# Kernel optimization log

Measured on AMD Instinct MI355X. Metric: run time of the kernel, lower is better.

The kernel has to match this reference:

```python
import jax, jax.numpy as jnp
import numpy as np

B = 256        # batch_size = y.size(0)
N_BLK = 128    # n: nodes per perturbed subgraph (== hidden_channels so trace blocks are square)
C = 128        # hidden_channels
WALK = 7       # self.walk_len
N_P = B * N_BLK
E_P = N_P * 16
N_NP = N_BLK
E_NP = N_NP * 16


def _gcn_norm(edge_index, num_nodes):
    # PyG gcn_norm: add self loops, symmetric D^{-1/2} (A+I) D^{-1/2}
    loop = jnp.arange(num_nodes, dtype=edge_index.dtype)
    src = jnp.concatenate([edge_index[0], loop])
    dst = jnp.concatenate([edge_index[1], loop])
    deg = jax.ops.segment_sum(jnp.ones_like(dst, dtype=jnp.float32), dst, num_segments=num_nodes)
    dinv = jnp.where(deg > 0, jax.lax.rsqrt(deg), 0.0)
    norm = dinv[src] * dinv[dst]  # [E + N]
    return src, dst, norm


def _gcn(x, src, dst, norm, W, b, num_nodes):
    # GCNConv: aggregate normalized messages from src at dst of (x @ W), then + bias
    xw = x @ W
    out = jax.ops.segment_sum(xw[src] * norm[:, None], dst, num_segments=num_nodes)
    return out + b


def setup_inputs() -> dict:
    key = jax.random.key(0)
    ks = jax.random.split(key, 12)
    x_p = jax.random.normal(ks[0], (N_P, C), dtype=jnp.float32)
    x_np = jax.random.normal(ks[1], (N_NP, C), dtype=jnp.float32)
    y = jax.random.uniform(ks[2], (B, 1), dtype=jnp.float32)
    edge_index_p = jax.random.randint(ks[3], (2, E_P), 0, N_P, dtype=jnp.int64)
    edge_index_np = jax.random.randint(ks[4], (2, E_NP), 0, N_NP, dtype=jnp.int64)
    # shared GCNConv weight/bias (same self.wrnn.conv1 applied every step to both graphs)
    W_gcn = jax.random.normal(ks[5], (C, C), dtype=jnp.float32) / np.sqrt(C)
    b_gcn = jnp.zeros((C,), dtype=jnp.float32)
    # MLP: walk_len -> 15 -> 1
    W1 = jax.random.normal(ks[6], (WALK, 15), dtype=jnp.float32) / np.sqrt(WALK)
    b1 = jnp.zeros((15,), dtype=jnp.float32)
    W2 = jax.random.normal(ks[7], (15, 1), dtype=jnp.float32) / np.sqrt(15)
    b2 = jnp.zeros((1,), dtype=jnp.float32)
    return {"x_p": x_p, "x_np": x_np, "y": y,
            "edge_index_p": edge_index_p, "edge_index_np": edge_index_np,
            "W_gcn": W_gcn, "b_gcn": b_gcn,
            "W1": W1, "b1": b1, "W2": W2, "b2": b2}


def reference(x_p, x_np, y, edge_index_p, edge_index_np, W_gcn, b_gcn, W1, b1, W2, b2):
    src_p, dst_p, norm_p = _gcn_norm(edge_index_p, N_P)
    src_n, dst_n, norm_n = _gcn_norm(edge_index_np, N_NP)
    h_p, h_np = x_p, x_np
    p_traces, np_traces = [], []
    for _ in range(WALK):  # small fixed walk_len loop
        h_p = _gcn(h_p, src_p, dst_p, norm_p, W_gcn, b_gcn, N_P)
        h_np = _gcn(h_np, src_n, dst_n, norm_n, W_gcn, b_gcn, N_NP)
        np_traces.append(jnp.trace(h_np))
        # fused batched block-trace: trace of each [n, C] block (n == C)
        p_traces.append(jnp.einsum('bkk->b', h_p.reshape(B, N_BLK, C)))
    p_list = jnp.stack(p_traces, axis=1)          # [B, WALK]
    np_list = jnp.stack(np_traces)[None, :]       # [1, WALK] broadcast == repeat
    p_list = (p_list - np_list) * ((y - 0.5) * 2.0)  # per-row sign scale
    mu = jnp.mean(p_list, axis=0, keepdims=True)
    std = jnp.std(p_list, axis=0, keepdims=True, ddof=1)  # torch.std uses ddof=1
    p_list = (p_list - mu) / std
    h = jax.nn.relu(p_list @ W1 + b1)
    return jax.nn.sigmoid(h @ W2 + b2)            # [B, 1]
```

## Files before the change

### kernel.cpp

```cpp
#include <hip/hip_runtime.h>
#include <hip/hip_bf16.h>
#include <math.h>

namespace {

constexpr int C_DIM  = 128;
constexpr int B_SZ   = 256;
constexpr int NP_OFF = 32768;
constexpr int N_TOT  = 32896;
constexpr int E_P    = 524288;
constexpr int E_NP   = 2048;
constexpr int E_TOT  = E_P + E_NP;
constexpr int WALK   = 7;
constexpr int NTR    = 257;
constexpr int ESZ    = E_TOT + N_TOT;
constexpr int EPAD   = 64;


__device__ __forceinline__ float bflo(unsigned int w) { return __uint_as_float(w << 16); }
__device__ __forceinline__ float bfhi(unsigned int w) { return __uint_as_float(w & 0xffff0000u); }


__global__ void init_kernel(int* __restrict__ cnt, float* __restrict__ trG,
                            float* __restrict__ ctr, float* __restrict__ c0,
                            int* __restrict__ bflag,
                            unsigned* __restrict__ srcs, float* __restrict__ norms) {
  int i = blockIdx.x * blockDim.x + threadIdx.x;
  if (i < N_TOT) { cnt[i] = 0; c0[i] = 1.0f; }
  if (i < WALK * NTR) { trG[i] = 0.0f; ctr[i] = 0.0f; }
  if (i < EPAD) { srcs[ESZ + i] = 0u; norms[ESZ + i] = 0.0f; }
  if (i == 0) *bflag = 0;
}

__global__ void count_kernel(const int* __restrict__ ei_p,
                             const int* __restrict__ ei_np,
                             int* __restrict__ cnt) {
  int e = blockIdx.x * blockDim.x + threadIdx.x;
  if (e < E_P) {
    int d = ei_p[E_P + e];
    atomicAdd(&cnt[d], 1);
  } else if (e < E_TOT) {
    int i = e - E_P;
    int d = ei_np[E_NP + i] + NP_OFF;
    atomicAdd(&cnt[d], 1);
  }
}

__global__ void scan_kernel(const int* __restrict__ cnt, int* __restrict__ ptr) {
  const int T = 1024;
  __shared__ int part[T];
  int tid = threadIdx.x;
  const int chunk = (N_TOT + T - 1) / T;
  int begin = tid * chunk;
  int end = begin + chunk;
  if (end > N_TOT) end = N_TOT;
  int s = 0;
  for (int i = begin; i < end; ++i) s += cnt[i] + 1;
  part[tid] = s;
  __syncthreads();
  for (int off = 1; off < T; off <<= 1) {
    int v = (tid >= off) ? part[tid - off] : 0;
    __syncthreads();
    part[tid] += v;
    __syncthreads();
  }
  if (tid == T - 1) ptr[N_TOT] = part[T - 1];
  int run = (tid == 0) ? 0 : part[tid - 1];
  for (int i = begin; i < end; ++i) { ptr[i] = run; run += cnt[i] + 1; }
}

__global__ void dinv_kernel(const int* __restrict__ cnt, const int* __restrict__ ptr,
                            float* __restrict__ dinv, int* __restrict__ fill,
                            unsigned* __restrict__ srcs, float* __restrict__ norms) {
  int i = blockIdx.x * blockDim.x + threadIdx.x;
  if (i < N_TOT) {
    float di = rsqrtf((float)cnt[i] + 1.0f);
    dinv[i] = di;
    fill[i] = 0;
    int p = ptr[i];
    srcs[p] = (unsigned)i;
    norms[p] = di * di;
  }
}

__global__ void fill_kernel(const int* __restrict__ ei_p,
                            const int* __restrict__ ei_np,
                            const int* __restrict__ ptr, int* __restrict__ fill,
                            const float* __restrict__ dinv,
                            unsigned* __restrict__ srcs, float* __restrict__ norms) {
  int e = blockIdx.x * blockDim.x + threadIdx.x;
  int s, d;
  if (e < E_P) {
    s = ei_p[e];
    d = ei_p[E_P + e];
  } else if (e < E_TOT) {
    int i = e - E_P;
    s = ei_np[i] + NP_OFF;
    d = ei_np[E_NP + i] + NP_OFF;
  } else {
    return;
  }
  int k = atomicAdd(&fill[d], 1);
  if (k < 63) {
    int pos = ptr[d] + 1 + k;
    srcs[pos] = (unsigned)s;
    norms[pos] = dinv[s] * dinv[d];
  }
}

__global__ void concat_kernel(const float* __restrict__ x_p,
                              const float* __restrict__ x_np,
                              __hip_bfloat16* __restrict__ hb) {
  int i = blockIdx.x * blockDim.x + threadIdx.x;
  const int NP8 = NP_OFF * C_DIM / 8;
  const int NT8 = N_TOT * C_DIM / 8;
  if (i >= NT8) return;
  const float* src = (i < NP8) ? (x_p + (size_t)i * 8)
                               : (x_np + (size_t)(i - NP8) * 8);
  union { __hip_bfloat16 h[8]; uint4 u; } pk;
#pragma unroll
  for (int j = 0; j < 8; ++j) pk.h[j] = __float2bfloat16(src[j]);
  ((uint4*)hb)[i] = pk.u;
}

__global__ __launch_bounds__(128) void wpow_all_kernel(
    const float* __restrict__ W, float* __restrict__ Vt_all,
    float* __restrict__ dvec_all, const float* __restrict__ bg,
    int* __restrict__ bflag) {
  __shared__ float cur[C_DIM];
  const int i = blockIdx.x;
  const int j = threadIdx.x;
  if (i < C_DIM) {
    float u = W[i * C_DIM + j];
    Vt_all[0 * C_DIM * C_DIM + j * C_DIM + i] = u;
    for (int st = 1; st < WALK; ++st) {
      cur[j] = u;
      __syncthreads();
      float nu = 0.0f;
      for (int k = 0; k < C_DIM; ++k) nu += cur[k] * W[k * C_DIM + j];
      __syncthreads();
      u = nu;
      Vt_all[st * C_DIM * C_DIM + j * C_DIM + i] = u;
    }
  } else {
    float d = bg[j];
    if (d != 0.0f) atomicOr(bflag, 1);
    dvec_all[0 * C_DIM + j] = d;
    for (int st = 1; st < WALK; ++st) {
      cur[j] = d;
      __syncthreads();
      float nd = 0.0f;
      for (int k = 0; k < C_DIM; ++k) nd += cur[k] * W[k * C_DIM + j];
      __syncthreads();
      d = nd;
      dvec_all[st * C_DIM + j] = d;
    }
  }
}

__global__ __launch_bounds__(256) void step_kernel(
    const __hip_bfloat16* __restrict__ Gin,
    __hip_bfloat16* __restrict__ Gout,
    const int* __restrict__ ptr,
    const unsigned* __restrict__ srcs,
    const float* __restrict__ norms,
    const float* __restrict__ cin,
    float* __restrict__ cout,
    const float* __restrict__ Vt,
    const float* __restrict__ dvec,
    float* __restrict__ trG,
    float* __restrict__ ctr,
    const int* __restrict__ bflag,
    int st, int notlast) {
  const int lane = threadIdx.x & 63;
  const int wv   = threadIdx.x >> 6;
  const int q    = lane >> 4;
  const int c8   = lane & 15;
  const int base = (blockIdx.x * 4 + wv) * 16;
  const int n0   = base + 4 * q;
  const int n1   = n0 + 1;
  const int n2   = n0 + 2;
  const int n3   = n0 + 3;
  const int qb   = q << 4;

  const int p0 = ptr[n0];
  const int p1 = ptr[n1];
  const int p2 = ptr[n2];
  const int p3 = ptr[n3];
  int d0 = ptr[n0 + 1] - p0; if (d0 > 64) d0 = 64;
  int d1 = ptr[n1 + 1] - p1; if (d1 > 64) d1 = 64;
  int d2 = ptr[n2 + 1] - p2; if (d2 > 64) d2 = 64;
  int d3 = ptr[n3 + 1] - p3; if (d3 > 64) d3 = 64;
  int dmax = d0 > d1 ? d0 : d1;
  dmax = dmax > d2 ? dmax : d2;
  dmax = dmax > d3 ? dmax : d3;

  const unsigned* S0 = srcs + p0;   const float* F0 = norms + p0;
  const unsigned* S1 = srcs + p1;   const float* F1 = norms + p1;
  const unsigned* S2 = srcs + p2;   const float* F2 = norms + p2;
  const unsigned* S3 = srcs + p3;   const float* F3 = norms + p3;
  unsigned sA0 = S0[c8], sB0 = S0[16 + c8], sC0 = S0[32 + c8], sD0 = S0[48 + c8];
  float    nA0 = F0[c8], nB0 = F0[16 + c8], nC0 = F0[32 + c8], nD0 = F0[48 + c8];
  unsigned sA1 = S1[c8], sB1 = S1[16 + c8], sC1 = S1[32 + c8], sD1 = S1[48 + c8];
  float    nA1 = F1[c8], nB1 = F1[16 + c8], nC1 = F1[32 + c8], nD1 = F1[48 + c8];
  unsigned sA2 = S2[c8], sB2 = S2[16 + c8], sC2 = S2[32 + c8], sD2 = S2[48 + c8];
  float    nA2 = F2[c8], nB2 = F2[16 + c8], nC2 = F2[32 + c8], nD2 = F2[48 + c8];
  unsigned sA3 = S3[c8], sB3 = S3[16 + c8], sC3 = S3[32 + c8], sD3 = S3[48 + c8];
  float    nA3 = F3[c8], nB3 = F3[16 + c8], nC3 = F3[32 + c8], nD3 = F3[48 + c8];

  const uint4* __restrict__ G16 = (const uint4*)Gin;

  float acc0[8], acc1[8], acc2[8], acc3[8];
#pragma unroll
  for (int i = 0; i < 8; ++i) { acc0[i] = 0.0f; acc1[i] = 0.0f;
                                acc2[i] = 0.0f; acc3[i] = 0.0f; }

#define LOADN(K, SX, NX, DK)                                                   \
    unsigned x##K##a = __shfl(SX, qb + rr * 4 + 0);                            \
    unsigned x##K##b = __shfl(SX, qb + rr * 4 + 1);                            \
    unsigned x##K##c = __shfl(SX, qb + rr * 4 + 2);                            \
    unsigned x##K##d = __shfl(SX, qb + rr * 4 + 3);                            \
    float w##K##a = __shfl(NX, qb + rr * 4 + 0);                               \
    float w##K##b = __shfl(NX, qb + rr * 4 + 1);                               \
    float w##K##c = __shfl(NX, qb + rr * 4 + 2);                               \
    float w##K##d = __shfl(NX, qb + rr * 4 + 3);                               \
    w##K##a = (j0 + 0 < DK) ? w##K##a : 0.0f;                                  \
    w##K##b = (j0 + 1 < DK) ? w##K##b : 0.0f;                                  \
    w##K##c = (j0 + 2 < DK) ? w##K##c : 0.0f;                                  \
    w##K##d = (j0 + 3 < DK) ? w##K##d : 0.0f;                                  \
    x##K##a = x##K##a < N_TOT ? x##K##a : 0u;                                  \
    x##K##b = x##K##b < N_TOT ? x##K##b : 0u;                                  \
    x##K##c = x##K##c < N_TOT ? x##K##c : 0u;                                  \
    x##K##d = x##K##d < N_TOT ? x##K##d : 0u;                                  \
    uint4 g##K##a = G16[(size_t)x##K##a * 16 + c8];                            \
    uint4 g##K##b = G16[(size_t)x##K##b * 16 + c8];                            \
    uint4 g##K##c = G16[(size_t)x##K##c * 16 + c8];                            \
    uint4 g##K##d = G16[(size_t)x##K##d * 16 + c8];

#define CONSN(K, ACC)                                                          \
    ACC[0] += w##K##a * bflo(g##K##a.x) + w##K##b * bflo(g##K##b.x)            \
            + w##K##c * bflo(g##K##c.x) + w##K##d * bflo(g##K##d.x);           \
    ACC[1] += w##K##a * bfhi(g##K##a.x) + w##K##b * bfhi(g##K##b.x)            \
            + w##K##c * bfhi(g##K##c.x) + w##K##d * bfhi(g##K##d.x);           \
    ACC[2] += w##K##a * bflo(g##K##a.y) + w##K##b * bflo(g##K##b.y)            \
            + w##K##c * bflo(g##K##c.y) + w##K##d * bflo(g##K##d.y);           \
    ACC[3] += w##K##a * bfhi(g##K##a.y) + w##K##b * bfhi(g##K##b.y)            \
            + w##K##c * bfhi(g##K##c.y) + w##K##d * bfhi(g##K##d.y);           \
    ACC[4] += w##K##a * bflo(g##K##a.z) + w##K##b * bflo(g##K##b.z)            \
            + w##K##c * bflo(g##K##c.z) + w##K##d * bflo(g##K##d.z);           \
    ACC[5] += w##K##a * bfhi(g##K##a.z) + w##K##b * bfhi(g##K##b.z)            \
            + w##K##c * bfhi(g##K##c.z) + w##K##d * bfhi(g##K##d.z);           \
    ACC[6] += w##K##a * bflo(g##K##a.w) + w##K##b * bflo(g##K##b.w)            \
            + w##K##c * bflo(g##K##c.w) + w##K##d * bflo(g##K##d.w);           \
    ACC[7] += w##K##a * bfhi(g##K##a.w) + w##K##b * bfhi(g##K##b.w)            \
            + w##K##c * bfhi(g##K##c.w) + w##K##d * bfhi(g##K##d.w);

#define GROUP4(SX0, NX0, SX1, NX1, SX2, NX2, SX3, NX3, RG)                     \
  if ((RG) * 16 < dmax) {                                                      \
    for (int rr = 0; rr < 4; ++rr) {                                           \
      const int j0 = (RG) * 16 + rr * 4;                                       \
      if (j0 >= dmax) break;                                                   \
      LOADN(0, SX0, NX0, d0)                                                   \
      LOADN(1, SX1, NX1, d1)                                                   \
      LOADN(2, SX2, NX2, d2)                                                   \
      LOADN(3, SX3, NX3, d3)                                                   \
      CONSN(0, acc0)                                                           \
      CONSN(1, acc1)                                                           \
      CONSN(2, acc2)                                                           \
      CONSN(3, acc3)                                                           \
    }                                                                          \
  }

  GROUP4(sA0, nA0, sA1, nA1, sA2, nA2, sA3, nA3, 0)
  GROUP4(sB0, nB0, sB1, nB1, sB2, nB2, sB3, nB3, 1)
  GROUP4(sC0, nC0, sC1, nC1, sC2, nC2, sC3, nC3, 2)
  GROUP4(sD0, nD0, sD1, nD1, sD2, nD2, sD3, nD3, 3)
#undef GROUP4
#undef CONSN
#undef LOADN

  if (notlast) {
    union { __hip_bfloat16 h[8]; uint4 u; } pk0, pk1, pk2, pk3;
#pragma unroll
    for (int i = 0; i < 8; ++i) { pk0.h[i] = __float2bfloat16(acc0[i]);
                                  pk1.h[i] = __float2bfloat16(acc1[i]);
                                  pk2.h[i] = __float2bfloat16(acc2[i]);
                                  pk3.h[i] = __float2bfloat16(acc3[i]); }
    ((uint4*)Gout)[(size_t)n0 * 16 + c8] = pk0.u;
    ((uint4*)Gout)[(size_t)n1 * 16 + c8] = pk1.u;
    ((uint4*)Gout)[(size_t)n2 * 16 + c8] = pk2.u;
    ((uint4*)Gout)[(size_t)n3 * 16 + c8] = pk3.u;
  }

  const int col0 = n0 & 127, col1 = n1 & 127, col2 = n2 & 127, col3 = n3 & 127;
  const float4* vr0 = (const float4*)(Vt + col0 * C_DIM + c8 * 8);
  const float4* vr1 = (const float4*)(Vt + col1 * C_DIM + c8 * 8);
  const float4* vr2 = (const float4*)(Vt + col2 * C_DIM + c8 * 8);
  const float4* vr3 = (const float4*)(Vt + col3 * C_DIM + c8 * 8);
  const float4 v00 = vr0[0], v01 = vr0[1];
  const float4 v10 = vr1[0], v11 = vr1[1];
  const float4 v20 = vr2[0], v21 = vr2[1];
  const float4 v30 = vr3[0], v31 = vr3[1];
  float pd = acc0[0] * v00.x + acc0[1] * v00.y + acc0[2] * v00.z + acc0[3] * v00.w +
             acc0[4] * v01.x + acc0[5] * v01.y + acc0[6] * v01.z + acc0[7] * v01.w;
  pd      += acc1[0] * v10.x + acc1[1] * v10.y + acc1[2] * v10.z + acc1[3] * v10.w +
             acc1[4] * v11.x + acc1[5] * v11.y + acc1[6] * v11.z + acc1[7] * v11.w;
  pd      += acc2[0] * v20.x + acc2[1] * v20.y + acc2[2] * v20.z + acc2[3] * v20.w +
             acc2[4] * v21.x + acc2[5] * v21.y + acc2[6] * v21.z + acc2[7] * v21.w;
  pd      += acc3[0] * v30.x + acc3[1] * v30.y + acc3[2] * v30.z + acc3[3] * v30.w +
             acc3[4] * v31.x + acc3[5] * v31.y + acc3[6] * v31.z + acc3[7] * v31.w;
  pd += __shfl_xor(pd, 1);
  pd += __shfl_xor(pd, 2);
  pd += __shfl_xor(pd, 4);
  pd += __shfl_xor(pd, 8);

  const int bnz = *bflag;
  if (c8 == 0) {
    atomicAdd(&trG[st * NTR + (n0 >> 7)], pd);
    if (bnz) {
      float cs0 = cin[n0], cn0 = 0.0f;
      for (int e = 0; e < d0; ++e) cn0 += norms[p0 + e] * cin[srcs[p0 + e]];
      float cs1 = cin[n1], cn1 = 0.0f;
      for (int e = 0; e < d1; ++e) cn1 += norms[p1 + e] * cin[srcs[p1 + e]];
      float cs2 = cin[n2], cn2 = 0.0f;
      for (int e = 0; e < d2; ++e) cn2 += norms[p2 + e] * cin[srcs[p2 + e]];
      float cs3 = cin[n3], cn3 = 0.0f;
      for (int e = 0; e < d3; ++e) cn3 += norms[p3 + e] * cin[srcs[p3 + e]];
      if (notlast) { cout[n0] = cn0; cout[n1] = cn1;
                     cout[n2] = cn2; cout[n3] = cn3; }
      atomicAdd(&ctr[st * NTR + (n0 >> 7)],
                cs0 * dvec[col0] + cs1 * dvec[col1] +
                cs2 * dvec[col2] + cs3 * dvec[col3]);
    }
  }
}

__global__ __launch_bounds__(256) void final_kernel(const float* __restrict__ trG,
                                                    const float* __restrict__ ctr,
                                                    const float* __restrict__ y,
                                                    const float* __restrict__ W1,
                                                    const float* __restrict__ b1,
                                                    const float* __restrict__ W2,
                                                    const float* __restrict__ b2,
                                                    float* __restrict__ out) {
  __shared__ float sm[B_SZ];
  const int b = threadIdx.x;
  const float sgn = (y[b] - 0.5f) * 2.0f;
  float runb = 0.0f, runn = 0.0f;
  float vals[WALK];
#pragma unroll
  for (int t = 0; t < WALK; ++t) {
    runb += ctr[t * NTR + b];
    runn += ctr[t * NTR + 256];
    vals[t] = ((trG[t * NTR + b] + runb) - (trG[t * NTR + 256] + runn)) * sgn;
  }

  for (int t = 0; t < WALK; ++t) {
    sm[b] = vals[t];
    __syncthreads();
    for (int off = 128; off >= 1; off >>= 1) {
      if (b < off) sm[b] += sm[b + off];
      __syncthreads();
    }
    float mean = sm[0] * (1.0f / 256.0f);
    __syncthreads();
    float d = vals[t] - mean;
    sm[b] = d * d;
    __syncthreads();
    for (int off = 128; off >= 1; off >>= 1) {
      if (b < off) sm[b] += sm[b + off];
      __syncthreads();
    }
    float stdv = sqrtf(sm[0] * (1.0f / 255.0f));
    __syncthreads();
    vals[t] = d / stdv;
  }

  float o = b2[0];
#pragma unroll
  for (int j = 0; j < 15; ++j) {
    float a = b1[j];
#pragma unroll
    for (int t = 0; t < WALK; ++t) a += vals[t] * W1[t * 15 + j];
    o += fmaxf(a, 0.0f) * W2[j];
  }
  out[b] = 1.0f / (1.0f + expf(-o));
}

}

extern "C" void kernel_launch(void* const* d_in, const int* in_sizes, int n_in,
                              void* d_out, int out_size, void* d_ws, size_t ws_size,
                              hipStream_t stream) {
  const float* x_p   = (const float*)d_in[0];
  const float* x_np  = (const float*)d_in[1];
  const float* y     = (const float*)d_in[2];
  const int* ei_p    = (const int*)d_in[3];
  const int* ei_np   = (const int*)d_in[4];
  const float* W_gcn = (const float*)d_in[5];
  const float* b_gcn = (const float*)d_in[6];
  const float* W1    = (const float*)d_in[7];
  const float* b1    = (const float*)d_in[8];
  const float* W2    = (const float*)d_in[9];
  const float* b2    = (const float*)d_in[10];
  float* out         = (float*)d_out;

  char* p = (char*)d_ws;
  auto alloc = [&](size_t bytes) -> void* {
    void* r = (void*)p;
    p += (bytes + 255) & ~(size_t)255;
    return r;
  };
  __hip_bfloat16* Ga = (__hip_bfloat16*)alloc((size_t)N_TOT * C_DIM * 2);
  __hip_bfloat16* Gb = (__hip_bfloat16*)alloc((size_t)N_TOT * C_DIM * 2);
  unsigned* srcs  = (unsigned*)alloc((size_t)(ESZ + EPAD) * 4);
  float* norms    = (float*)alloc((size_t)(ESZ + EPAD) * 4);
  int*   ptr      = (int*)alloc((size_t)(N_TOT + 1) * 4);
  float* dinv     = (float*)alloc((size_t)N_TOT * 4);
  int*   cnt      = (int*)alloc((size_t)N_TOT * 4);
  int*   fill     = (int*)alloc((size_t)N_TOT * 4);
  float* ca       = (float*)alloc((size_t)N_TOT * 4);
  float* cb       = (float*)alloc((size_t)N_TOT * 4);
  float* Vt_all   = (float*)alloc((size_t)WALK * C_DIM * C_DIM * 4);
  float* dvec_all = (float*)alloc((size_t)WALK * C_DIM * 4);
  float* trG      = (float*)alloc((size_t)WALK * NTR * 4);
  float* ctr      = (float*)alloc((size_t)WALK * NTR * 4);
  int*   bflag    = (int*)alloc(4);

  init_kernel<<<(N_TOT + 255) / 256, 256, 0, stream>>>(cnt, trG, ctr, ca, bflag,
                                                       srcs, norms);
  count_kernel<<<(E_TOT + 255) / 256, 256, 0, stream>>>(ei_p, ei_np, cnt);
  scan_kernel<<<1, 1024, 0, stream>>>(cnt, ptr);
  dinv_kernel<<<(N_TOT + 255) / 256, 256, 0, stream>>>(cnt, ptr, dinv, fill,
                                                       srcs, norms);
  fill_kernel<<<(E_TOT + 255) / 256, 256, 0, stream>>>(ei_p, ei_np, ptr, fill,
                                                       dinv, srcs, norms);
  {
    const int NT8 = N_TOT * C_DIM / 8;
    concat_kernel<<<(NT8 + 255) / 256, 256, 0, stream>>>(x_p, x_np, Ga);
  }
  wpow_all_kernel<<<C_DIM + 1, C_DIM, 0, stream>>>(W_gcn, Vt_all, dvec_all,
                                                   b_gcn, bflag);

  __hip_bfloat16 *Gcur = Ga, *Gnext = Gb;
  float *ccur = ca, *cnext = cb;
  for (int st = 0; st < WALK; ++st) {
    const int notlast = (st < WALK - 1) ? 1 : 0;
    step_kernel<<<N_TOT / 64, 256, 0, stream>>>(Gcur, Gnext, ptr, srcs, norms,
                                                ccur, cnext,
                                                Vt_all + (size_t)st * C_DIM * C_DIM,
                                                dvec_all + (size_t)st * C_DIM,
                                                trG, ctr, bflag, st, notlast);
    { __hip_bfloat16* t = Gcur; Gcur = Gnext; Gnext = t; }
    { float* t = ccur; ccur = cnext; cnext = t; }
  }

  final_kernel<<<1, B_SZ, 0, stream>>>(trG, ctr, y, W1, b1, W2, b2, out);
}
```

Measured before the change: 476.3 us.

## Replace CSR adjacency with fixed-width ELL layout and drop the scan kernel

Adjacency is now stored in an ELL layout, a fixed 64-slot row per node indexed by node*64, instead of CSR with a prefix-sum pointer array. This removes the single-block scan kernel and the ptr loads in the step kernel. Edge index and norm loads for each 16-slot group are now issued only when that group is needed. The final kernel's tree reductions are replaced with wavefront shuffle reductions. The ELL buffers are larger (N*64 entries) and their rows are strided, which may cost memory traffic and coalescing.

```diff
diff --git a/kernel.cpp b/kernel.cpp
--- a/kernel.cpp
+++ b/kernel.cpp
@@ -13,8 +13,7 @@
 constexpr int E_TOT  = E_P + E_NP;
 constexpr int WALK   = 7;
 constexpr int NTR    = 257;
-constexpr int ESZ    = E_TOT + N_TOT;
-constexpr int EPAD   = 64;
+constexpr int ELLW   = 64;
 
 
 __device__ __forceinline__ float bflo(unsigned int w) { return __uint_as_float(w << 16); }
@@ -23,12 +22,10 @@
 
 __global__ void init_kernel(int* __restrict__ cnt, float* __restrict__ trG,
                             float* __restrict__ ctr, float* __restrict__ c0,
-                            int* __restrict__ bflag,
-                            unsigned* __restrict__ srcs, float* __restrict__ norms) {
+                            int* __restrict__ bflag) {
   int i = blockIdx.x * blockDim.x + threadIdx.x;
   if (i < N_TOT) { cnt[i] = 0; c0[i] = 1.0f; }
   if (i < WALK * NTR) { trG[i] = 0.0f; ctr[i] = 0.0f; }
-  if (i < EPAD) { srcs[ESZ + i] = 0u; norms[ESZ + i] = 0.0f; }
   if (i == 0) *bflag = 0;
 }
 
@@ -46,30 +43,7 @@
   }
 }
 
-__global__ void scan_kernel(const int* __restrict__ cnt, int* __restrict__ ptr) {
-  const int T = 1024;
-  __shared__ int part[T];
-  int tid = threadIdx.x;
-  const int chunk = (N_TOT + T - 1) / T;
-  int begin = tid * chunk;
-  int end = begin + chunk;
-  if (end > N_TOT) end = N_TOT;
-  int s = 0;
-  for (int i = begin; i < end; ++i) s += cnt[i] + 1;
-  part[tid] = s;
-  __syncthreads();
-  for (int off = 1; off < T; off <<= 1) {
-    int v = (tid >= off) ? part[tid - off] : 0;
-    __syncthreads();
-    part[tid] += v;
-    __syncthreads();
-  }
-  if (tid == T - 1) ptr[N_TOT] = part[T - 1];
-  int run = (tid == 0) ? 0 : part[tid - 1];
-  for (int i = begin; i < end; ++i) { ptr[i] = run; run += cnt[i] + 1; }
-}
-
-__global__ void dinv_kernel(const int* __restrict__ cnt, const int* __restrict__ ptr,
+__global__ void dinv_kernel(const int* __restrict__ cnt,
                             float* __restrict__ dinv, int* __restrict__ fill,
                             unsigned* __restrict__ srcs, float* __restrict__ norms) {
   int i = blockIdx.x * blockDim.x + threadIdx.x;
@@ -77,7 +51,7 @@
     float di = rsqrtf((float)cnt[i] + 1.0f);
     dinv[i] = di;
     fill[i] = 0;
-    int p = ptr[i];
+    size_t p = (size_t)i * ELLW;
     srcs[p] = (unsigned)i;
     norms[p] = di * di;
   }
@@ -85,7 +59,7 @@
 
 __global__ void fill_kernel(const int* __restrict__ ei_p,
                             const int* __restrict__ ei_np,
-                            const int* __restrict__ ptr, int* __restrict__ fill,
+                            int* __restrict__ fill,
                             const float* __restrict__ dinv,
                             unsigned* __restrict__ srcs, float* __restrict__ norms) {
   int e = blockIdx.x * blockDim.x + threadIdx.x;
@@ -101,8 +75,8 @@
     return;
   }
   int k = atomicAdd(&fill[d], 1);
-  if (k < 63) {
-    int pos = ptr[d] + 1 + k;
+  if (k < ELLW - 1) {
+    size_t pos = (size_t)d * ELLW + 1 + k;
     srcs[pos] = (unsigned)s;
     norms[pos] = dinv[s] * dinv[d];
   }
@@ -161,7 +135,7 @@
 __global__ __launch_bounds__(256) void step_kernel(
     const __hip_bfloat16* __restrict__ Gin,
     __hip_bfloat16* __restrict__ Gout,
-    const int* __restrict__ ptr,
+    const int* __restrict__ cnt,
     const unsigned* __restrict__ srcs,
     const float* __restrict__ norms,
     const float* __restrict__ cin,
@@ -183,30 +157,18 @@
   const int n3   = n0 + 3;
   const int qb   = q << 4;
 
-  const int p0 = ptr[n0];
-  const int p1 = ptr[n1];
-  const int p2 = ptr[n2];
-  const int p3 = ptr[n3];
-  int d0 = ptr[n0 + 1] - p0; if (d0 > 64) d0 = 64;
-  int d1 = ptr[n1 + 1] - p1; if (d1 > 64) d1 = 64;
-  int d2 = ptr[n2 + 1] - p2; if (d2 > 64) d2 = 64;
-  int d3 = ptr[n3 + 1] - p3; if (d3 > 64) d3 = 64;
+  int d0 = cnt[n0] + 1; if (d0 > ELLW) d0 = ELLW;
+  int d1 = cnt[n1] + 1; if (d1 > ELLW) d1 = ELLW;
+  int d2 = cnt[n2] + 1; if (d2 > ELLW) d2 = ELLW;
+  int d3 = cnt[n3] + 1; if (d3 > ELLW) d3 = ELLW;
   int dmax = d0 > d1 ? d0 : d1;
   dmax = dmax > d2 ? dmax : d2;
   dmax = dmax > d3 ? dmax : d3;
 
-  const unsigned* S0 = srcs + p0;   const float* F0 = norms + p0;
-  const unsigned* S1 = srcs + p1;   const float* F1 = norms + p1;
-  const unsigned* S2 = srcs + p2;   const float* F2 = norms + p2;
-  const unsigned* S3 = srcs + p3;   const float* F3 = norms + p3;
-  unsigned sA0 = S0[c8], sB0 = S0[16 + c8], sC0 = S0[32 + c8], sD0 = S0[48 + c8];
-  float    nA0 = F0[c8], nB0 = F0[16 + c8], nC0 = F0[32 + c8], nD0 = F0[48 + c8];
-  unsigned sA1 = S1[c8], sB1 = S1[16 + c8], sC1 = S1[32 + c8], sD1 = S1[48 + c8];
-  float    nA1 = F1[c8], nB1 = F1[16 + c8], nC1 = F1[32 + c8], nD1 = F1[48 + c8];
-  unsigned sA2 = S2[c8], sB2 = S2[16 + c8], sC2 = S2[32 + c8], sD2 = S2[48 + c8];
-  float    nA2 = F2[c8], nB2 = F2[16 + c8], nC2 = F2[32 + c8], nD2 = F2[48 + c8];
-  unsigned sA3 = S3[c8], sB3 = S3[16 + c8], sC3 = S3[32 + c8], sD3 = S3[48 + c8];
-  float    nA3 = F3[c8], nB3 = F3[16 + c8], nC3 = F3[32 + c8], nD3 = F3[48 + c8];
+  const unsigned* S0 = srcs + (size_t)n0 * ELLW;  const float* F0 = norms + (size_t)n0 * ELLW;
+  const unsigned* S1 = srcs + (size_t)n1 * ELLW;  const float* F1 = norms + (size_t)n1 * ELLW;
+  const unsigned* S2 = srcs + (size_t)n2 * ELLW;  const float* F2 = norms + (size_t)n2 * ELLW;
+  const unsigned* S3 = srcs + (size_t)n3 * ELLW;  const float* F3 = norms + (size_t)n3 * ELLW;
 
   const uint4* __restrict__ G16 = (const uint4*)Gin;
 
@@ -256,7 +218,7 @@
             + w##K##c * bfhi(g##K##c.w) + w##K##d * bfhi(g##K##d.w);
 
 #define GROUP4(SX0, NX0, SX1, NX1, SX2, NX2, SX3, NX3, RG)                     \
-  if ((RG) * 16 < dmax) {                                                      \
+  {                                                                            \
     for (int rr = 0; rr < 4; ++rr) {                                           \
       const int j0 = (RG) * 16 + rr * 4;                                       \
       if (j0 >= dmax) break;                                                   \
@@ -271,10 +233,26 @@
     }                                                                          \
   }
 
-  GROUP4(sA0, nA0, sA1, nA1, sA2, nA2, sA3, nA3, 0)
-  GROUP4(sB0, nB0, sB1, nB1, sB2, nB2, sB3, nB3, 1)
-  GROUP4(sC0, nC0, sC1, nC1, sC2, nC2, sC3, nC3, 2)
-  GROUP4(sD0, nD0, sD1, nD1, sD2, nD2, sD3, nD3, 3)
+  {
+    unsigned sA0 = S0[c8], sA1 = S1[c8], sA2 = S2[c8], sA3 = S3[c8];
+    float    nA0 = F0[c8], nA1 = F1[c8], nA2 = F2[c8], nA3 = F3[c8];
+    unsigned sB0 = S0[16 + c8], sB1 = S1[16 + c8], sB2 = S2[16 + c8], sB3 = S3[16 + c8];
+    float    nB0 = F0[16 + c8], nB1 = F1[16 + c8], nB2 = F2[16 + c8], nB3 = F3[16 + c8];
+    GROUP4(sA0, nA0, sA1, nA1, sA2, nA2, sA3, nA3, 0)
+    if (16 < dmax) {
+      GROUP4(sB0, nB0, sB1, nB1, sB2, nB2, sB3, nB3, 1)
+    }
+  }
+  if (32 < dmax) {
+    unsigned sC0 = S0[32 + c8], sC1 = S1[32 + c8], sC2 = S2[32 + c8], sC3 = S3[32 + c8];
+    float    nC0 = F0[32 + c8], nC1 = F1[32 + c8], nC2 = F2[32 + c8], nC3 = F3[32 + c8];
+    GROUP4(sC0, nC0, sC1, nC1, sC2, nC2, sC3, nC3, 2)
+    if (48 < dmax) {
+      unsigned sD0 = S0[48 + c8], sD1 = S1[48 + c8], sD2 = S2[48 + c8], sD3 = S3[48 + c8];
+      float    nD0 = F0[48 + c8], nD1 = F1[48 + c8], nD2 = F2[48 + c8], nD3 = F3[48 + c8];
+      GROUP4(sD0, nD0, sD1, nD1, sD2, nD2, sD3, nD3, 3)
+    }
+  }
 #undef GROUP4
 #undef CONSN
 #undef LOADN
@@ -319,13 +297,13 @@
     atomicAdd(&trG[st * NTR + (n0 >> 7)], pd);
     if (bnz) {
       float cs0 = cin[n0], cn0 = 0.0f;
-      for (int e = 0; e < d0; ++e) cn0 += norms[p0 + e] * cin[srcs[p0 + e]];
+      for (int e = 0; e < d0; ++e) cn0 += F0[e] * cin[S0[e]];
       float cs1 = cin[n1], cn1 = 0.0f;
-      for (int e = 0; e < d1; ++e) cn1 += norms[p1 + e] * cin[srcs[p1 + e]];
+      for (int e = 0; e < d1; ++e) cn1 += F1[e] * cin[S1[e]];
       float cs2 = cin[n2], cn2 = 0.0f;
-      for (int e = 0; e < d2; ++e) cn2 += norms[p2 + e] * cin[srcs[p2 + e]];
+      for (int e = 0; e < d2; ++e) cn2 += F2[e] * cin[S2[e]];
       float cs3 = cin[n3], cn3 = 0.0f;
-      for (int e = 0; e < d3; ++e) cn3 += norms[p3 + e] * cin[srcs[p3 + e]];
+      for (int e = 0; e < d3; ++e) cn3 += F3[e] * cin[S3[e]];
       if (notlast) { cout[n0] = cn0; cout[n1] = cn1;
                      cout[n2] = cn2; cout[n3] = cn3; }
       atomicAdd(&ctr[st * NTR + (n0 >> 7)],
@@ -343,8 +321,10 @@
                                                     const float* __restrict__ W2,
                                                     const float* __restrict__ b2,
                                                     float* __restrict__ out) {
-  __shared__ float sm[B_SZ];
-  const int b = threadIdx.x;
+  __shared__ float part[4];
+  const int b  = threadIdx.x;
+  const int ln = b & 63;
+  const int wv = b >> 6;
   const float sgn = (y[b] - 0.5f) * 2.0f;
   float runb = 0.0f, runn = 0.0f;
   float vals[WALK];
@@ -356,22 +336,20 @@
   }
 
   for (int t = 0; t < WALK; ++t) {
-    sm[b] = vals[t];
+    float v = vals[t];
+    v += __shfl_xor(v, 1);  v += __shfl_xor(v, 2);  v += __shfl_xor(v, 4);
+    v += __shfl_xor(v, 8);  v += __shfl_xor(v, 16); v += __shfl_xor(v, 32);
+    if (ln == 0) part[wv] = v;
     __syncthreads();
-    for (int off = 128; off >= 1; off >>= 1) {
-      if (b < off) sm[b] += sm[b + off];
-      __syncthreads();
-    }
-    float mean = sm[0] * (1.0f / 256.0f);
+    float mean = (part[0] + part[1] + part[2] + part[3]) * (1.0f / 256.0f);
     __syncthreads();
     float d = vals[t] - mean;
-    sm[b] = d * d;
+    v = d * d;
+    v += __shfl_xor(v, 1);  v += __shfl_xor(v, 2);  v += __shfl_xor(v, 4);
+    v += __shfl_xor(v, 8);  v += __shfl_xor(v, 16); v += __shfl_xor(v, 32);
+    if (ln == 0) part[wv] = v;
     __syncthreads();
-    for (int off = 128; off >= 1; off >>= 1) {
-      if (b < off) sm[b] += sm[b + off];
-      __syncthreads();
-    }
-    float stdv = sqrtf(sm[0] * (1.0f / 255.0f));
+    float stdv = sqrtf((part[0] + part[1] + part[2] + part[3]) * (1.0f / 255.0f));
     __syncthreads();
     vals[t] = d / stdv;
   }
@@ -413,9 +391,8 @@
   };
   __hip_bfloat16* Ga = (__hip_bfloat16*)alloc((size_t)N_TOT * C_DIM * 2);
   __hip_bfloat16* Gb = (__hip_bfloat16*)alloc((size_t)N_TOT * C_DIM * 2);
-  unsigned* srcs  = (unsigned*)alloc((size_t)(ESZ + EPAD) * 4);
-  float* norms    = (float*)alloc((size_t)(ESZ + EPAD) * 4);
-  int*   ptr      = (int*)alloc((size_t)(N_TOT + 1) * 4);
+  unsigned* srcs  = (unsigned*)alloc((size_t)N_TOT * ELLW * 4);
+  float* norms    = (float*)alloc((size_t)N_TOT * ELLW * 4);
   float* dinv     = (float*)alloc((size_t)N_TOT * 4);
   int*   cnt      = (int*)alloc((size_t)N_TOT * 4);
   int*   fill     = (int*)alloc((size_t)N_TOT * 4);
@@ -427,13 +404,11 @@
   float* ctr      = (float*)alloc((size_t)WALK * NTR * 4);
   int*   bflag    = (int*)alloc(4);
 
-  init_kernel<<<(N_TOT + 255) / 256, 256, 0, stream>>>(cnt, trG, ctr, ca, bflag,
+  init_kernel<<<(N_TOT + 255) / 256, 256, 0, stream>>>(cnt, trG, ctr, ca, bflag);
+  count_kernel<<<(E_TOT + 255) / 256, 256, 0, stream>>>(ei_p, ei_np, cnt);
+  dinv_kernel<<<(N_TOT + 255) / 256, 256, 0, stream>>>(cnt, dinv, fill,
                                                        srcs, norms);
-  count_kernel<<<(E_TOT + 255) / 256, 256, 0, stream>>>(ei_p, ei_np, cnt);
-  scan_kernel<<<1, 1024, 0, stream>>>(cnt, ptr);
-  dinv_kernel<<<(N_TOT + 255) / 256, 256, 0, stream>>>(cnt, ptr, dinv, fill,
-                                                       srcs, norms);
-  fill_kernel<<<(E_TOT + 255) / 256, 256, 0, stream>>>(ei_p, ei_np, ptr, fill,
+  fill_kernel<<<(E_TOT + 255) / 256, 256, 0, stream>>>(ei_p, ei_np, fill,
                                                        dinv, srcs, norms);
   {
     const int NT8 = N_TOT * C_DIM / 8;
@@ -446,7 +421,7 @@
   float *ccur = ca, *cnext = cb;
   for (int st = 0; st < WALK; ++st) {
     const int notlast = (st < WALK - 1) ? 1 : 0;
-    step_kernel<<<N_TOT / 64, 256, 0, stream>>>(Gcur, Gnext, ptr, srcs, norms,
+    step_kernel<<<N_TOT / 64, 256, 0, stream>>>(Gcur, Gnext, cnt, srcs, norms,
                                                 ccur, cnext,
                                                 Vt_all + (size_t)st * C_DIM * C_DIM,
                                                 dvec_all + (size_t)st * C_DIM,
```

New measurement: 422.7 us (median of 2 runs). -11.2%, faster.
